# Optimization experiments

Hardware: AMD Instinct MI355X
Metric: run time of the kernel (lower is better)

## Reference

```python
import jax, jax.numpy as jnp
import numpy as np

DIM = 1024
HEADS = 16
DIM_HEAD = 64
SEQ = 2048
BATCH = 2
SCALE = DIM_HEAD ** -0.5
NEG = -jnp.finfo(jnp.float32).max


def setup_inputs() -> dict:
    key = jax.random.key(0)
    k1, k2, k3 = jax.random.split(key, 3)
    x = jax.random.normal(k1, (BATCH, SEQ, DIM), dtype=jnp.float32)
    w_qkv = jax.random.normal(k2, (DIM, 3 * HEADS * DIM_HEAD), dtype=jnp.float32) * 0.02
    w_out = jax.random.normal(k3, (HEADS * DIM_HEAD, DIM), dtype=jnp.float32) * 0.02
    b_out = jnp.zeros((DIM,), dtype=jnp.float32)
    return {"x": x, "w_qkv": w_qkv, "w_out": w_out, "b_out": b_out}


def reference(x, w_qkv, w_out, b_out):
    b, n, _ = x.shape
    qkv = x @ w_qkv  # [b, n, 3*h*d]
    q, k, v = jnp.split(qkv, 3, axis=-1)
    def to_heads(t):
        return t.reshape(b, n, HEADS, DIM_HEAD).transpose(0, 2, 1, 3)  # b h n d
    q, k, v = to_heads(q), to_heads(k), to_heads(v)
    q = q * SCALE
    dots = jnp.einsum('bhid,bhjd->bhij', q, k)  # materialized [b,h,n,n] scores
    causal_mask = jnp.triu(jnp.ones((n, n), dtype=bool), k=1)
    dots = jnp.where(causal_mask, NEG, dots)
    attn = jax.nn.softmax(dots, axis=-1)
    out = jnp.einsum('bhij,bhjd->bhid', attn, v)
    out = out.transpose(0, 2, 1, 3).reshape(b, n, HEADS * DIM_HEAD)
    return out @ w_out + b_out
```

## Files before the change

kernel.cpp:

```cpp
#include <hip/hip_runtime.h>
#include <cstdint>

typedef __attribute__((ext_vector_type(8))) short bfrag_t;
typedef __attribute__((ext_vector_type(4))) float f32x4_t;

#define MFMA16(a,b,c) __builtin_amdgcn_mfma_f32_16x16x32_bf16((a),(b),(c),0,0,0)

__device__ __forceinline__ unsigned short f2bf(float f){
  unsigned u = __float_as_uint(f);
  unsigned r = u + 0x7fffu + ((u >> 16) & 1u);
  return (unsigned short)(r >> 16);
}

__device__ __forceinline__ unsigned pk2bf(float a, float b){
  unsigned r;
  asm("v_cvt_pk_bf16_f32 %0, %1, %2" : "=v"(r) : "v"(a), "v"(b));
  return r;
}

__device__ __forceinline__ void gload16(const unsigned short* g, unsigned short* l){
  __builtin_amdgcn_global_load_lds(
      (const __attribute__((address_space(1))) unsigned int*)(const void*)g,
      (__attribute__((address_space(3))) unsigned int*)(void*)l,
      16, 0, 0);
}

__global__ __launch_bounds__(256) void k_prep(
    const float* __restrict__ x,     unsigned short* __restrict__ xbf,
    const float* __restrict__ wqkv,  unsigned short* __restrict__ wqkvT,
    const float* __restrict__ wout,  unsigned short* __restrict__ woutT)
{
  __shared__ unsigned short tile[32][33];
  const int bid = blockIdx.x;
  const int tid = threadIdx.x;

  if (bid < 2048){
    const int n4 = 4096*1024/4;
    int i = bid*256 + tid;
    #pragma unroll
    for(int it=0; it<2; it++, i += 2048*256){
      if (i < n4){
        float4 v = ((const float4*)x)[i];
        ushort4 o;
        o.x = f2bf(v.x); o.y = f2bf(v.y); o.z = f2bf(v.z); o.w = f2bf(v.w);
        ((ushort4*)xbf)[i] = o;
      }
    }
    return;
  }

  const float* in; unsigned short* out; int R, C, idx;
  if (bid < 5120){ in = wqkv; out = wqkvT; R = 1024; C = 3072; idx = bid - 2048; }
  else           { in = wout; out = woutT; R = 1024; C = 1024; idx = bid - 5120; }
  const int nbc = C >> 5;
  const int bc = (idx % nbc) * 32, br = (idx / nbc) * 32;
  const int tx = tid & 31, ty = tid >> 5;
  #pragma unroll
  for(int i=0;i<32;i+=8){
    tile[ty+i][tx] = f2bf(in[(size_t)(br+ty+i)*C + bc + tx]);
  }
  __syncthreads();
  #pragma unroll
  for(int i=0;i<32;i+=8){
    out[(size_t)(bc+ty+i)*R + br + tx] = tile[tx][ty+i];
  }
}

__global__ __launch_bounds__(256) void k_gemm1(
    const unsigned short* __restrict__ A,
    const unsigned short* __restrict__ Bt,
    unsigned short* __restrict__ Qo, unsigned short* __restrict__ Kimg,
    unsigned short* __restrict__ Vimg)
{
  __shared__ unsigned short ldsA[128*64];
  __shared__ unsigned short ldsB[128*64];

  const int tid = threadIdx.x;
  const int lane = tid & 63;
  const int w = tid >> 6;
  const int wr = w >> 1, wc = w & 1;
  const int col16 = lane & 15, g = lane >> 4;

  const int L = blockIdx.x;
  const int swz = (L & 7) * 96 + (L >> 3);
  const int bm = (swz / 24) * 128;
  const int bn = (swz % 24) * 128;
  const int K = 1024;
  const int SWAP = (bn < 2048) ? 1 : 0;

  f32x4_t acc[4][4];
  #pragma unroll
  for(int i=0;i<4;i++)
    #pragma unroll
    for(int j=0;j<4;j++) acc[i][j] = (f32x4_t)0.0f;

  for(int k0=0; k0<K; k0+=64){
    __syncthreads();
    #pragma unroll
    for(int i=0; i<4; i++){
      int u = i*256 + tid;
      int row = u>>3, s = u&7, gs = s ^ (row&7);
      gload16(A + (size_t)(bm+row)*K + k0 + gs*8, ldsA + (i*256 + w*64)*8);
    }
    #pragma unroll
    for(int i=0; i<4; i++){
      int u = i*256 + tid;
      int row = u>>3, s = u&7, gs = s ^ (row&7);
      gload16(Bt + (size_t)(bn+row)*K + k0 + gs*8, ldsB + (i*256 + w*64)*8);
    }
    __syncthreads();
    #pragma unroll
    for(int kk=0; kk<2; kk++){
      bfrag_t af[4], bfr[4];
      #pragma unroll
      for(int mi=0;mi<4;mi++){
        int row = wr*64 + mi*16 + col16;
        int slot = (kk*4 + g) ^ (row&7);
        af[mi] = *(const bfrag_t*)(ldsA + row*64 + slot*8);
      }
      #pragma unroll
      for(int ni=0;ni<4;ni++){
        int row = wc*64 + ni*16 + col16;
        int slot = (kk*4 + g) ^ (row&7);
        bfr[ni] = *(const bfrag_t*)(ldsB + row*64 + slot*8);
      }
      if (SWAP){
        #pragma unroll
        for(int mi=0;mi<4;mi++)
          #pragma unroll
          for(int ni=0;ni<4;ni++)
            acc[mi][ni] = MFMA16(bfr[ni], af[mi], acc[mi][ni]);
      } else {
        #pragma unroll
        for(int mi=0;mi<4;mi++)
          #pragma unroll
          for(int ni=0;ni<4;ni++)
            acc[mi][ni] = MFMA16(af[mi], bfr[ni], acc[mi][ni]);
      }
    }
  }

  if (bn < 2048){
    const int which = bn >> 10;
    #pragma unroll
    for(int mi=0;mi<4;mi++){
      int s_full = bm + wr*64 + mi*16 + col16;
      int b = s_full >> 11, sq = s_full & 2047;
      #pragma unroll
      for(int ni=0;ni<4;ni++){
        int n0 = bn + wc*64 + ni*16 + g*4;
        int h = (n0 & 1023) >> 6;
        int d0 = n0 & 63;
        size_t bh = (size_t)(b*16 + h);
        float v0 = acc[mi][ni][0], v1 = acc[mi][ni][1];
        float v2 = acc[mi][ni][2], v3 = acc[mi][ni][3];
        if (which == 0){
          const float sc = 0.18033688f;
          uint2 pkd; pkd.x = pk2bf(v0*sc, v1*sc); pkd.y = pk2bf(v2*sc, v3*sc);
          *(uint2*)(Qo + (bh*2048 + sq)*64 + d0) = pkd;
        } else {
          int kt = sq >> 6, rr = sq & 63;
          int ks = rr >> 4, c16i = rr & 15;
          int dk = d0 >> 5, g3 = (d0 >> 3) & 3, e0 = d0 & 7;
          uint2 pkd; pkd.x = pk2bf(v0, v1); pkd.y = pk2bf(v2, v3);
          size_t off = bh*131072 + (size_t)kt*4096
                     + (size_t)(ks*2 + dk)*512 + (size_t)(g3*16 + c16i)*8 + e0;
          *(uint2*)(Kimg + off) = pkd;
        }
      }
    }
  } else {
    #pragma unroll
    for(int mi=0;mi<4;mi++){
      int s0 = bm + wr*64 + mi*16 + g*4;
      int b = s0 >> 11, sq0 = s0 & 2047;
      int kt = sq0 >> 6, sc0 = sq0 & 63;
      int jk = sc0 >> 5, g3 = (sc0 >> 3) & 3, e0 = sc0 & 7;
      #pragma unroll
      for(int ni=0;ni<4;ni++){
        int ncol = bn + wc*64 + ni*16 + col16;
        int h = (ncol & 1023) >> 6;
        int d64 = ncol & 63;
        int nimg = d64 >> 4, c16i = d64 & 15;
        size_t bh = (size_t)(b*16 + h);
        uint2 pkd;
        pkd.x = pk2bf(acc[mi][ni][0], acc[mi][ni][1]);
        pkd.y = pk2bf(acc[mi][ni][2], acc[mi][ni][3]);
        size_t off = bh*131072 + (size_t)kt*4096
                   + (size_t)(nimg*2 + jk)*512 + (size_t)(g3*16 + c16i)*8 + e0;
        *(uint2*)(Vimg + off) = pkd;
      }
    }
  }
}

__global__ __launch_bounds__(256) void k_gemm2(
    const unsigned short* __restrict__ A,
    const unsigned short* __restrict__ Bt,
    float* __restrict__ Co, const float* __restrict__ bias)
{
  __shared__ unsigned short ldsA[64*64];
  __shared__ unsigned short ldsB[128*64];

  const int tid = threadIdx.x;
  const int lane = tid & 63;
  const int w = tid >> 6;
  const int wc = w;
  const int col16 = lane & 15, g = lane >> 4;

  const int L = blockIdx.x;
  const int swz = (L & 7) * 64 + (L >> 3);
  const int bm = (swz >> 3) * 64;
  const int bn = (swz & 7) * 128;
  const int K = 1024, N = 1024;

  f32x4_t acc[4][2];
  #pragma unroll
  for(int i=0;i<4;i++)
    #pragma unroll
    for(int j=0;j<2;j++) acc[i][j] = (f32x4_t)0.0f;

  for(int k0=0; k0<K; k0+=64){
    __syncthreads();
    #pragma unroll
    for(int i=0; i<2; i++){
      int u = i*256 + tid;
      int row = u>>3, s = u&7, gs = s ^ (row&7);
      gload16(A + (size_t)(bm+row)*K + k0 + gs*8, ldsA + (i*256 + w*64)*8);
    }
    #pragma unroll
    for(int i=0; i<4; i++){
      int u = i*256 + tid;
      int row = u>>3, s = u&7, gs = s ^ (row&7);
      gload16(Bt + (size_t)(bn+row)*K + k0 + gs*8, ldsB + (i*256 + w*64)*8);
    }
    __syncthreads();
    #pragma unroll
    for(int kk=0; kk<2; kk++){
      bfrag_t af[4], bfr[2];
      #pragma unroll
      for(int mi=0;mi<4;mi++){
        int row = mi*16 + col16;
        int slot = (kk*4 + g) ^ (row&7);
        af[mi] = *(const bfrag_t*)(ldsA + row*64 + slot*8);
      }
      #pragma unroll
      for(int ni=0;ni<2;ni++){
        int row = wc*32 + ni*16 + col16;
        int slot = (kk*4 + g) ^ (row&7);
        bfr[ni] = *(const bfrag_t*)(ldsB + row*64 + slot*8);
      }
      #pragma unroll
      for(int mi=0;mi<4;mi++)
        #pragma unroll
        for(int ni=0;ni<2;ni++)
          acc[mi][ni] = MFMA16(af[mi], bfr[ni], acc[mi][ni]);
    }
  }

  #pragma unroll
  for(int mi=0;mi<4;mi++){
    int mrow = bm + mi*16 + g*4;
    #pragma unroll
    for(int ni=0;ni<2;ni++){
      int ncol = bn + wc*32 + ni*16 + col16;
      float bb = bias[ncol];
      #pragma unroll
      for(int r=0;r<4;r++){
        Co[(size_t)(mrow+r)*N + ncol] = acc[mi][ni][r] + bb;
      }
    }
  }
}

__global__ __launch_bounds__(256, 4) void k_attn(
    const unsigned short* __restrict__ Q,
    const unsigned short* __restrict__ Kimg,
    const unsigned short* __restrict__ Vimg,
    unsigned short* __restrict__ O)
{
  __shared__ unsigned short kls[2*4096];
  __shared__ unsigned short vls[2*4096];
  __shared__ unsigned short plds[4*1024];
  const int lane = threadIdx.x & 63;
  const int w = threadIdx.x >> 6;
  const int col16 = lane & 15, g = lane >> 4;
  const int bh = blockIdx.x;
  const int y = blockIdx.y;
  const int idx = (y & 7)*4 + (y >> 3);
  const int qt = (idx & 1) ? (31 - (idx >> 1)) : (idx >> 1);
  const int b = bh >> 4, h = bh & 15;

  const unsigned short* Qb = Q    + (size_t)bh*2048*64;
  const unsigned short* Kb = Kimg + (size_t)bh*131072;
  const unsigned short* Vb = Vimg + (size_t)bh*131072;
  char* pw = (char*)(plds + w*1024);

  auto stage = [&](int kt, int bsel){
    const unsigned short* gk = Kb + (size_t)kt*4096;
    const unsigned short* gv = Vb + (size_t)kt*4096;
    unsigned short* lk = kls + bsel*4096;
    unsigned short* lv = vls + bsel*4096;
    #pragma unroll
    for(int c=0;c<2;c++){
      int chunk = w*2 + c;
      int u = chunk*64 + lane;
      gload16(gk + u*8, lk + chunk*512);
      gload16(gv + u*8, lv + chunk*512);
    }
  };

  const int qrow0 = qt*64 + w*16;
  const int nkt = qt + 1;
  const int qi = qrow0 + col16;

  bfrag_t qf[2];
  #pragma unroll
  for(int dk=0;dk<2;dk++)
    qf[dk] = *(const bfrag_t*)(Qb + (size_t)(qrow0 + col16)*64 + dk*32 + g*8);

  f32x4_t oaccT[4];
  #pragma unroll
  for(int n=0;n<4;n++) oaccT[n] = (f32x4_t)0.0f;
  float mrun = -1e30f, lrun = 0.f;

  stage(0, 0);
  __syncthreads();

  #pragma unroll 1
  for(int kt=0; kt<nkt; kt++){
    const int cur = kt & 1;
    if (kt+1 < nkt) stage(kt+1, cur^1);

    const bfrag_t* kb = (const bfrag_t*)(kls + cur*4096);
    const bfrag_t* vb = (const bfrag_t*)(vls + cur*4096);

    f32x4_t sacc[4];
    __builtin_amdgcn_s_setprio(1);
    #pragma unroll
    for(int ks=0; ks<4; ks++){
      bfrag_t kf0 = kb[(ks*2+0)*64 + lane];
      bfrag_t kf1 = kb[(ks*2+1)*64 + lane];
      f32x4_t c = (f32x4_t)0.0f;
      c = MFMA16(kf0, qf[0], c);
      c = MFMA16(kf1, qf[1], c);
      sacc[ks] = c;
    }
    __builtin_amdgcn_s_setprio(0);
    if (kt == qt){
      const int kbase = kt*64;
      #pragma unroll
      for(int ks=0; ks<4; ks++)
        #pragma unroll
        for(int r=0;r<4;r++){
          int kj = kbase + ks*16 + g*4 + r;
          if (kj > qi) sacc[ks][r] = -1e30f;
        }
    }
    float pm = fmaxf(
        fmaxf(fmaxf(fmaxf(sacc[0][0],sacc[0][1]),fmaxf(sacc[0][2],sacc[0][3])),
              fmaxf(fmaxf(sacc[1][0],sacc[1][1]),fmaxf(sacc[1][2],sacc[1][3]))),
        fmaxf(fmaxf(fmaxf(sacc[2][0],sacc[2][1]),fmaxf(sacc[2][2],sacc[2][3])),
              fmaxf(fmaxf(sacc[3][0],sacc[3][1]),fmaxf(sacc[3][2],sacc[3][3]))));
    pm = fmaxf(pm, __shfl_xor(pm, 16));
    pm = fmaxf(pm, __shfl_xor(pm, 32));
    if (!__all(pm - mrun <= 11.5415603f)){
      float mnew = fmaxf(mrun, pm);
      float alpha = __builtin_amdgcn_exp2f(mrun - mnew);
      mrun = mnew;
      lrun *= alpha;
      #pragma unroll
      for(int n=0;n<4;n++)
        #pragma unroll
        for(int r=0;r<4;r++)
          oaccT[n][r] *= alpha;
    }
    float rs = 0.f;
    #pragma unroll
    for(int ks=0; ks<4; ks++){
      float p0 = __builtin_amdgcn_exp2f(sacc[ks][0] - mrun);
      float p1 = __builtin_amdgcn_exp2f(sacc[ks][1] - mrun);
      float p2 = __builtin_amdgcn_exp2f(sacc[ks][2] - mrun);
      float p3 = __builtin_amdgcn_exp2f(sacc[ks][3] - mrun);
      rs += (p0+p1)+(p2+p3);
      unsigned w0 = pk2bf(p0, p1);
      unsigned w1 = pk2bf(p2, p3);
      int byte0 = (col16*128 + (ks*16 + g*4)*2) ^ ((col16&7)<<4);
      unsigned long long wd = ((unsigned long long)w1 << 32) | w0;
      *(unsigned long long*)(pw + byte0) = wd;
    }
    rs += __shfl_xor(rs, 16);
    rs += __shfl_xor(rs, 32);
    lrun += rs;
    bfrag_t pf[2];
    #pragma unroll
    for(int jk=0;jk<2;jk++){
      int byteo = (col16*128 + jk*64 + g*16) ^ ((col16&7)<<4);
      pf[jk] = *(const bfrag_t*)(pw + byteo);
    }
    __builtin_amdgcn_s_setprio(1);
    #pragma unroll
    for(int n=0;n<4;n++){
      bfrag_t v0 = vb[(n*2+0)*64 + lane];
      bfrag_t v1 = vb[(n*2+1)*64 + lane];
      oaccT[n] = MFMA16(v0, pf[0], oaccT[n]);
      oaccT[n] = MFMA16(v1, pf[1], oaccT[n]);
    }
    __builtin_amdgcn_s_setprio(0);
    __syncthreads();
  }

  {
    float inv = 1.0f / lrun;
    size_t obase = ((size_t)(b*2048 + qi))*1024 + (size_t)h*64;
    #pragma unroll
    for(int n=0;n<4;n++){
      uint2 pkd;
      pkd.x = pk2bf(oaccT[n][0]*inv, oaccT[n][1]*inv);
      pkd.y = pk2bf(oaccT[n][2]*inv, oaccT[n][3]*inv);
      *(uint2*)(O + obase + n*16 + g*4) = pkd;
    }
  }
}

extern "C" void kernel_launch(void* const* d_in, const int* in_sizes, int n_in,
                              void* d_out, int out_size, void* d_ws, size_t ws_size,
                              hipStream_t stream){
  const float* x     = (const float*)d_in[0];
  const float* w_qkv = (const float*)d_in[1];
  const float* w_out = (const float*)d_in[2];
  const float* b_out = (const float*)d_in[3];
  float* out = (float*)d_out;

  unsigned char* ws = (unsigned char*)d_ws;
  unsigned short* xbf   = (unsigned short*)(ws);
  unsigned short* wqkvT = (unsigned short*)(ws + (size_t)8*1024*1024);
  unsigned short* woutT = (unsigned short*)(ws + (size_t)14*1024*1024);
  unsigned short* Qb    = (unsigned short*)(ws + (size_t)16*1024*1024);
  unsigned short* Kb    = (unsigned short*)(ws + (size_t)24*1024*1024);
  unsigned short* Vtb   = (unsigned short*)(ws + (size_t)32*1024*1024);
  unsigned short* attno = xbf;

  k_prep<<<6144, 256, 0, stream>>>(x, xbf, w_qkv, wqkvT, w_out, woutT);
  k_gemm1<<<768, 256, 0, stream>>>(xbf, wqkvT, Qb, Kb, Vtb);
  k_attn<<<dim3(32, 32), 256, 0, stream>>>(Qb, Kb, Vtb, attno);
  k_gemm2<<<512, 256, 0, stream>>>(attno, woutT, out, b_out);
}
```

Before: 111.5 us.

## Double-buffer QKV GEMM LDS tiles with fine-grained staged prefetch

Rewrites the QKV projection GEMM main loop to use two LDS buffers per operand. Each K-step's loads are split into quarter stages interleaved with MFMA quadrants, using explicit vmcnt waits, barriers and s_setprio, so global loads overlap compute. It also drops the block-index swizzle for L2 locality, which may reduce cache reuse. LDS usage doubles to 64KB, which could lower occupancy.

```diff
diff --git a/kernel.cpp b/kernel.cpp
--- a/kernel.cpp
+++ b/kernel.cpp
@@ -72,8 +72,10 @@
     unsigned short* __restrict__ Qo, unsigned short* __restrict__ Kimg,
     unsigned short* __restrict__ Vimg)
 {
-  __shared__ unsigned short ldsA[128*64];
-  __shared__ unsigned short ldsB[128*64];
+  __shared__ unsigned short lA0[128*64];
+  __shared__ unsigned short lA1[128*64];
+  __shared__ unsigned short lB0[128*64];
+  __shared__ unsigned short lB1[128*64];
 
   const int tid = threadIdx.x;
   const int lane = tid & 63;
@@ -82,10 +84,8 @@
   const int col16 = lane & 15, g = lane >> 4;
 
   const int L = blockIdx.x;
-  const int swz = (L & 7) * 96 + (L >> 3);
-  const int bm = (swz / 24) * 128;
-  const int bn = (swz % 24) * 128;
-  const int K = 1024;
+  const int bm = (L / 24) * 128;
+  const int bn = (L % 24) * 128;
   const int SWAP = (bn < 2048) ? 1 : 0;
 
   f32x4_t acc[4][4];
@@ -94,51 +94,88 @@
     #pragma unroll
     for(int j=0;j<4;j++) acc[i][j] = (f32x4_t)0.0f;
 
-  for(int k0=0; k0<K; k0+=64){
-    __syncthreads();
-    #pragma unroll
-    for(int i=0; i<4; i++){
-      int u = i*256 + tid;
-      int row = u>>3, s = u&7, gs = s ^ (row&7);
-      gload16(A + (size_t)(bm+row)*K + k0 + gs*8, ldsA + (i*256 + w*64)*8);
-    }
-    #pragma unroll
-    for(int i=0; i<4; i++){
-      int u = i*256 + tid;
-      int row = u>>3, s = u&7, gs = s ^ (row&7);
-      gload16(Bt + (size_t)(bn+row)*K + k0 + gs*8, ldsB + (i*256 + w*64)*8);
-    }
-    __syncthreads();
-    #pragma unroll
-    for(int kk=0; kk<2; kk++){
-      bfrag_t af[4], bfr[4];
-      #pragma unroll
-      for(int mi=0;mi<4;mi++){
-        int row = wr*64 + mi*16 + col16;
-        int slot = (kk*4 + g) ^ (row&7);
-        af[mi] = *(const bfrag_t*)(ldsA + row*64 + slot*8);
-      }
-      #pragma unroll
-      for(int ni=0;ni<4;ni++){
-        int row = wc*64 + ni*16 + col16;
-        int slot = (kk*4 + g) ^ (row&7);
-        bfr[ni] = *(const bfrag_t*)(ldsB + row*64 + slot*8);
-      }
-      if (SWAP){
-        #pragma unroll
-        for(int mi=0;mi<4;mi++)
-          #pragma unroll
-          for(int ni=0;ni<4;ni++)
-            acc[mi][ni] = MFMA16(bfr[ni], af[mi], acc[mi][ni]);
-      } else {
-        #pragma unroll
-        for(int mi=0;mi<4;mi++)
-          #pragma unroll
-          for(int ni=0;ni<4;ni++)
-            acc[mi][ni] = MFMA16(af[mi], bfr[ni], acc[mi][ni]);
-      }
-    }
-  }
+  bfrag_t af[4][2], bfp[2][2];
+
+#define STAGE_HALF(SRCPTR, ROWOFF, DSTARR, ODD, K0)                            \
+  { int r0_ = (ODD)*32 + (tid>>3);                                             \
+    gload16((SRCPTR) + (size_t)((ROWOFF)+r0_)*1024 + (K0) + ((tid&7)^(r0_&7))*8,\
+            (DSTARR) + ((ODD)*256 + w*64)*8);                                  \
+    int r1_ = 64 + (ODD)*32 + (tid>>3);                                        \
+    gload16((SRCPTR) + (size_t)((ROWOFF)+r1_)*1024 + (K0) + ((tid&7)^(r1_&7))*8,\
+            (DSTARR) + (512 + (ODD)*256 + w*64)*8); }
+
+#define RDF(ARR, ROWBASE, KK)                                                  \
+  (*(const bfrag_t*)((ARR) + ((ROWBASE)+col16)*64 +                            \
+                     ((((KK)*4+g) ^ (((ROWBASE)+col16)&7))*8)))
+
+#define MMQ(M0, N0)                                                            \
+  __builtin_amdgcn_s_setprio(1);                                               \
+  if (SWAP){                                                                   \
+    _Pragma("unroll") for(int mi_=0;mi_<2;mi_++)                               \
+    _Pragma("unroll") for(int nj_=0;nj_<2;nj_++)                               \
+    _Pragma("unroll") for(int kk_=0;kk_<2;kk_++)                               \
+      acc[(M0)+mi_][(N0)+nj_] =                                                \
+        MFMA16(bfp[nj_][kk_], af[(M0)+mi_][kk_], acc[(M0)+mi_][(N0)+nj_]);     \
+  } else {                                                                     \
+    _Pragma("unroll") for(int mi_=0;mi_<2;mi_++)                               \
+    _Pragma("unroll") for(int nj_=0;nj_<2;nj_++)                               \
+    _Pragma("unroll") for(int kk_=0;kk_<2;kk_++)                               \
+      acc[(M0)+mi_][(N0)+nj_] =                                                \
+        MFMA16(af[(M0)+mi_][kk_], bfp[nj_][kk_], acc[(M0)+mi_][(N0)+nj_]);     \
+  }                                                                            \
+  __builtin_amdgcn_s_setprio(0);
+
+#define KSTEP(RA, RB, WA, WB, KN, W0S, W1S, W2S, DOSTAGE)                      \
+  {                                                                            \
+    asm volatile(W0S ::: "memory");                                            \
+    asm volatile("s_barrier" ::: "memory");                                    \
+    if (DOSTAGE){ STAGE_HALF(A, bm, WA, 0, KN); }                              \
+    af[0][0]=RDF(RA, wr*64+ 0, 0); af[0][1]=RDF(RA, wr*64+ 0, 1);              \
+    af[1][0]=RDF(RA, wr*64+16, 0); af[1][1]=RDF(RA, wr*64+16, 1);              \
+    bfp[0][0]=RDF(RB, wc*64+ 0, 0); bfp[0][1]=RDF(RB, wc*64+ 0, 1);            \
+    bfp[1][0]=RDF(RB, wc*64+16, 0); bfp[1][1]=RDF(RB, wc*64+16, 1);            \
+    MMQ(0,0);                                                                  \
+    asm volatile(W1S ::: "memory");                                            \
+    asm volatile("s_barrier" ::: "memory");                                    \
+    if (DOSTAGE){ STAGE_HALF(Bt, bn, WB, 0, KN); }                             \
+    af[2][0]=RDF(RA, wr*64+32, 0); af[2][1]=RDF(RA, wr*64+32, 1);              \
+    af[3][0]=RDF(RA, wr*64+48, 0); af[3][1]=RDF(RA, wr*64+48, 1);              \
+    MMQ(2,0);                                                                  \
+    asm volatile(W2S ::: "memory");                                            \
+    asm volatile("s_barrier" ::: "memory");                                    \
+    if (DOSTAGE){ STAGE_HALF(A, bm, WA, 1, KN); }                              \
+    bfp[0][0]=RDF(RB, wc*64+32, 0); bfp[0][1]=RDF(RB, wc*64+32, 1);            \
+    bfp[1][0]=RDF(RB, wc*64+48, 0); bfp[1][1]=RDF(RB, wc*64+48, 1);            \
+    MMQ(0,2);                                                                  \
+    asm volatile("s_barrier" ::: "memory");                                    \
+    if (DOSTAGE){ STAGE_HALF(Bt, bn, WB, 1, KN); }                             \
+    MMQ(2,2);                                                                  \
+  }
+
+  STAGE_HALF(A, bm, lA0, 0, 0);
+  STAGE_HALF(Bt, bn, lB0, 0, 0);
+  STAGE_HALF(A, bm, lA0, 1, 0);
+  STAGE_HALF(Bt, bn, lB0, 1, 0);
+
+  #pragma unroll 1
+  for(int s8=0; s8<7; s8++){
+    const int kn1 = (2*s8+1)*64;
+    const int kn2 = (2*s8+2)*64;
+    KSTEP(lA0, lB0, lA1, lB1, kn1,
+          "s_waitcnt vmcnt(4)", "s_waitcnt vmcnt(4)", "s_waitcnt vmcnt(4)", true);
+    KSTEP(lA1, lB1, lA0, lB0, kn2,
+          "s_waitcnt vmcnt(4)", "s_waitcnt vmcnt(4)", "s_waitcnt vmcnt(4)", true);
+  }
+  KSTEP(lA0, lB0, lA1, lB1, 15*64,
+        "s_waitcnt vmcnt(4)", "s_waitcnt vmcnt(4)", "s_waitcnt vmcnt(4)", true);
+  KSTEP(lA1, lB1, lA0, lB0, 0,
+        "s_waitcnt vmcnt(4)", "s_waitcnt vmcnt(2)", "s_waitcnt vmcnt(0)", false);
+  asm volatile("s_waitcnt vmcnt(0)" ::: "memory");
+
+#undef KSTEP
+#undef MMQ
+#undef RDF
+#undef STAGE_HALF
 
   if (bn < 2048){
     const int which = bn >> 10;
```

After: 112.3 us. Within noise of the previous version (+0.7%).

## Pair adjacent query tiles per 512-thread attention block to share K/V staging

Applied to the files above, without the earlier changes.

The attention kernel now runs 8 waves per block, each half handling one of two adjacent 64-row query tiles, so K/V tiles staged in LDS are shared by both query tiles and each wave issues half the global loads. Blocks are ordered by y so that heavy and light tile pairs interleave, and waves of the lower tile skip compute once past their causal range while still joining the barriers. The GEMM1 block swizzle is also removed in favour of plain row-major tile order. The change trades halved K/V traffic for idle waves on the last tile, fewer and larger blocks, and possibly worse L2 locality in GEMM1.

```diff
diff --git a/kernel.cpp b/kernel.cpp
--- a/kernel.cpp
+++ b/kernel.cpp
@@ -82,9 +82,8 @@
   const int col16 = lane & 15, g = lane >> 4;
 
   const int L = blockIdx.x;
-  const int swz = (L & 7) * 96 + (L >> 3);
-  const int bm = (swz / 24) * 128;
-  const int bn = (swz % 24) * 128;
+  const int bm = (L / 24) * 128;
+  const int bn = (L % 24) * 128;
   const int K = 1024;
   const int SWAP = (bn < 2048) ? 1 : 0;
 
@@ -273,7 +272,7 @@
   }
 }
 
-__global__ __launch_bounds__(256, 4) void k_attn(
+__global__ __launch_bounds__(512, 2) void k_attn(
     const unsigned short* __restrict__ Q,
     const unsigned short* __restrict__ Kimg,
     const unsigned short* __restrict__ Vimg,
@@ -281,14 +280,16 @@
 {
   __shared__ unsigned short kls[2*4096];
   __shared__ unsigned short vls[2*4096];
-  __shared__ unsigned short plds[4*1024];
-  const int lane = threadIdx.x & 63;
-  const int w = threadIdx.x >> 6;
+  __shared__ unsigned short plds[8*1024];
+  const int tid = threadIdx.x;
+  const int lane = tid & 63;
+  const int w = tid >> 6;
+  const int wl = w & 3;
   const int col16 = lane & 15, g = lane >> 4;
   const int bh = blockIdx.x;
   const int y = blockIdx.y;
-  const int idx = (y & 7)*4 + (y >> 3);
-  const int qt = (idx & 1) ? (31 - (idx >> 1)) : (idx >> 1);
+  const int qt2 = (y < 8) ? y : (23 - y);
+  const int qt = qt2*2 + (w >> 2);
   const int b = bh >> 4, h = bh & 15;
 
   const unsigned short* Qb = Q    + (size_t)bh*2048*64;
@@ -301,23 +302,19 @@
     const unsigned short* gv = Vb + (size_t)kt*4096;
     unsigned short* lk = kls + bsel*4096;
     unsigned short* lv = vls + bsel*4096;
-    #pragma unroll
-    for(int c=0;c<2;c++){
-      int chunk = w*2 + c;
-      int u = chunk*64 + lane;
-      gload16(gk + u*8, lk + chunk*512);
-      gload16(gv + u*8, lv + chunk*512);
-    }
+    int u = w*64 + lane;
+    gload16(gk + u*8, lk + w*512);
+    gload16(gv + u*8, lv + w*512);
   };
 
-  const int qrow0 = qt*64 + w*16;
-  const int nkt = qt + 1;
+  const int qrow0 = qt*64 + wl*16;
   const int qi = qrow0 + col16;
+  const int nktb = 2*qt2 + 2;
 
   bfrag_t qf[2];
   #pragma unroll
   for(int dk=0;dk<2;dk++)
-    qf[dk] = *(const bfrag_t*)(Qb + (size_t)(qrow0 + col16)*64 + dk*32 + g*8);
+    qf[dk] = *(const bfrag_t*)(Qb + (size_t)qi*64 + dk*32 + g*8);
 
   f32x4_t oaccT[4];
   #pragma unroll
@@ -328,85 +325,87 @@
   __syncthreads();
 
   #pragma unroll 1
-  for(int kt=0; kt<nkt; kt++){
+  for(int kt=0; kt<nktb; kt++){
     const int cur = kt & 1;
-    if (kt+1 < nkt) stage(kt+1, cur^1);
-
-    const bfrag_t* kb = (const bfrag_t*)(kls + cur*4096);
-    const bfrag_t* vb = (const bfrag_t*)(vls + cur*4096);
-
-    f32x4_t sacc[4];
-    __builtin_amdgcn_s_setprio(1);
-    #pragma unroll
-    for(int ks=0; ks<4; ks++){
-      bfrag_t kf0 = kb[(ks*2+0)*64 + lane];
-      bfrag_t kf1 = kb[(ks*2+1)*64 + lane];
-      f32x4_t c = (f32x4_t)0.0f;
-      c = MFMA16(kf0, qf[0], c);
-      c = MFMA16(kf1, qf[1], c);
-      sacc[ks] = c;
-    }
-    __builtin_amdgcn_s_setprio(0);
-    if (kt == qt){
-      const int kbase = kt*64;
-      #pragma unroll
-      for(int ks=0; ks<4; ks++)
+    if (kt+1 < nktb) stage(kt+1, cur^1);
+
+    if (kt <= qt){
+      const bfrag_t* kb = (const bfrag_t*)(kls + cur*4096);
+      const bfrag_t* vb = (const bfrag_t*)(vls + cur*4096);
+
+      f32x4_t sacc[4];
+      __builtin_amdgcn_s_setprio(1);
+      #pragma unroll
+      for(int ks=0; ks<4; ks++){
+        bfrag_t kf0 = kb[(ks*2+0)*64 + lane];
+        bfrag_t kf1 = kb[(ks*2+1)*64 + lane];
+        f32x4_t c = (f32x4_t)0.0f;
+        c = MFMA16(kf0, qf[0], c);
+        c = MFMA16(kf1, qf[1], c);
+        sacc[ks] = c;
+      }
+      __builtin_amdgcn_s_setprio(0);
+      if (kt == qt){
+        const int kbase = kt*64;
         #pragma unroll
-        for(int r=0;r<4;r++){
-          int kj = kbase + ks*16 + g*4 + r;
-          if (kj > qi) sacc[ks][r] = -1e30f;
-        }
-    }
-    float pm = fmaxf(
-        fmaxf(fmaxf(fmaxf(sacc[0][0],sacc[0][1]),fmaxf(sacc[0][2],sacc[0][3])),
-              fmaxf(fmaxf(sacc[1][0],sacc[1][1]),fmaxf(sacc[1][2],sacc[1][3]))),
-        fmaxf(fmaxf(fmaxf(sacc[2][0],sacc[2][1]),fmaxf(sacc[2][2],sacc[2][3])),
-              fmaxf(fmaxf(sacc[3][0],sacc[3][1]),fmaxf(sacc[3][2],sacc[3][3]))));
-    pm = fmaxf(pm, __shfl_xor(pm, 16));
-    pm = fmaxf(pm, __shfl_xor(pm, 32));
-    if (!__all(pm - mrun <= 11.5415603f)){
-      float mnew = fmaxf(mrun, pm);
-      float alpha = __builtin_amdgcn_exp2f(mrun - mnew);
-      mrun = mnew;
-      lrun *= alpha;
-      #pragma unroll
-      for(int n=0;n<4;n++)
+        for(int ks=0; ks<4; ks++)
+          #pragma unroll
+          for(int r=0;r<4;r++){
+            int kj = kbase + ks*16 + g*4 + r;
+            if (kj > qi) sacc[ks][r] = -1e30f;
+          }
+      }
+      float pm = fmaxf(
+          fmaxf(fmaxf(fmaxf(sacc[0][0],sacc[0][1]),fmaxf(sacc[0][2],sacc[0][3])),
+                fmaxf(fmaxf(sacc[1][0],sacc[1][1]),fmaxf(sacc[1][2],sacc[1][3]))),
+          fmaxf(fmaxf(fmaxf(sacc[2][0],sacc[2][1]),fmaxf(sacc[2][2],sacc[2][3])),
+                fmaxf(fmaxf(sacc[3][0],sacc[3][1]),fmaxf(sacc[3][2],sacc[3][3]))));
+      pm = fmaxf(pm, __shfl_xor(pm, 16));
+      pm = fmaxf(pm, __shfl_xor(pm, 32));
+      if (!__all(pm - mrun <= 11.5415603f)){
+        float mnew = fmaxf(mrun, pm);
+        float alpha = __builtin_amdgcn_exp2f(mrun - mnew);
+        mrun = mnew;
+        lrun *= alpha;
         #pragma unroll
-        for(int r=0;r<4;r++)
-          oaccT[n][r] *= alpha;
-    }
-    float rs = 0.f;
-    #pragma unroll
-    for(int ks=0; ks<4; ks++){
-      float p0 = __builtin_amdgcn_exp2f(sacc[ks][0] - mrun);
-      float p1 = __builtin_amdgcn_exp2f(sacc[ks][1] - mrun);
-      float p2 = __builtin_amdgcn_exp2f(sacc[ks][2] - mrun);
-      float p3 = __builtin_amdgcn_exp2f(sacc[ks][3] - mrun);
-      rs += (p0+p1)+(p2+p3);
-      unsigned w0 = pk2bf(p0, p1);
-      unsigned w1 = pk2bf(p2, p3);
-      int byte0 = (col16*128 + (ks*16 + g*4)*2) ^ ((col16&7)<<4);
-      unsigned long long wd = ((unsigned long long)w1 << 32) | w0;
-      *(unsigned long long*)(pw + byte0) = wd;
-    }
-    rs += __shfl_xor(rs, 16);
-    rs += __shfl_xor(rs, 32);
-    lrun += rs;
-    bfrag_t pf[2];
-    #pragma unroll
-    for(int jk=0;jk<2;jk++){
-      int byteo = (col16*128 + jk*64 + g*16) ^ ((col16&7)<<4);
-      pf[jk] = *(const bfrag_t*)(pw + byteo);
-    }
-    __builtin_amdgcn_s_setprio(1);
-    #pragma unroll
-    for(int n=0;n<4;n++){
-      bfrag_t v0 = vb[(n*2+0)*64 + lane];
-      bfrag_t v1 = vb[(n*2+1)*64 + lane];
-      oaccT[n] = MFMA16(v0, pf[0], oaccT[n]);
-      oaccT[n] = MFMA16(v1, pf[1], oaccT[n]);
-    }
-    __builtin_amdgcn_s_setprio(0);
+        for(int n=0;n<4;n++)
+          #pragma unroll
+          for(int r=0;r<4;r++)
+            oaccT[n][r] *= alpha;
+      }
+      float rs = 0.f;
+      #pragma unroll
+      for(int ks=0; ks<4; ks++){
+        float p0 = __builtin_amdgcn_exp2f(sacc[ks][0] - mrun);
+        float p1 = __builtin_amdgcn_exp2f(sacc[ks][1] - mrun);
+        float p2 = __builtin_amdgcn_exp2f(sacc[ks][2] - mrun);
+        float p3 = __builtin_amdgcn_exp2f(sacc[ks][3] - mrun);
+        rs += (p0+p1)+(p2+p3);
+        unsigned w0 = pk2bf(p0, p1);
+        unsigned w1 = pk2bf(p2, p3);
+        int byte0 = (col16*128 + (ks*16 + g*4)*2) ^ ((col16&7)<<4);
+        unsigned long long wd = ((unsigned long long)w1 << 32) | w0;
+        *(unsigned long long*)(pw + byte0) = wd;
+      }
+      rs += __shfl_xor(rs, 16);
+      rs += __shfl_xor(rs, 32);
+      lrun += rs;
+      bfrag_t pf[2];
+      #pragma unroll
+      for(int jk=0;jk<2;jk++){
+        int byteo = (col16*128 + jk*64 + g*16) ^ ((col16&7)<<4);
+        pf[jk] = *(const bfrag_t*)(pw + byteo);
+      }
+      __builtin_amdgcn_s_setprio(1);
+      #pragma unroll
+      for(int n=0;n<4;n++){
+        bfrag_t v0 = vb[(n*2+0)*64 + lane];
+        bfrag_t v1 = vb[(n*2+1)*64 + lane];
+        oaccT[n] = MFMA16(v0, pf[0], oaccT[n]);
+        oaccT[n] = MFMA16(v1, pf[1], oaccT[n]);
+      }
+      __builtin_amdgcn_s_setprio(0);
+    }
     __syncthreads();
   }
 
@@ -443,6 +442,6 @@
 
   k_prep<<<6144, 256, 0, stream>>>(x, xbf, w_qkv, wqkvT, w_out, woutT);
   k_gemm1<<<768, 256, 0, stream>>>(xbf, wqkvT, Qb, Kb, Vtb);
-  k_attn<<<dim3(32, 32), 256, 0, stream>>>(Qb, Kb, Vtb, attno);
+  k_attn<<<dim3(32, 16), 512, 0, stream>>>(Qb, Kb, Vtb, attno);
   k_gemm2<<<512, 256, 0, stream>>>(attno, woutT, out, b_out);
 }
```

Result: slower. 113.9 us (+2.2%).
